# Optimization experiments

Measured on AMD Instinct MI355X. Metric: run time of the kernel, lower is better.

The kernel has to match this reference:

```python
import jax, jax.numpy as jnp
import numpy as np

B, S, H = 2, 2048, 2048
NH, KVH, HD = 32, 8, 64
G = NH // KVH
BASE = 10000.0
SCALE = 1.0 / np.sqrt(HD).astype(np.float32)


def _rope_cache(seq_len, dim, base):
    inv_freq = 1.0 / (base ** (jnp.arange(0, dim, 2, dtype=jnp.float32) / dim))
    t = jnp.arange(seq_len, dtype=jnp.float32)
    freqs = jnp.outer(t, inv_freq)            # [S, HD/2]
    emb = jnp.concatenate([freqs, freqs], -1)  # [S, HD]
    return jnp.cos(emb), jnp.sin(emb)


def _rotate_half(x):
    x1, x2 = jnp.split(x, 2, axis=-1)
    return jnp.concatenate([-x2, x1], axis=-1)


def setup_inputs() -> dict:
    key = jax.random.key(0)
    ks = jax.random.split(key, 5)
    hidden_states = jax.random.normal(ks[0], (B, S, H), jnp.float32)
    # additive causal mask, broadcast over heads
    causal = jnp.tril(jnp.ones((S, S), dtype=bool))
    attention_mask = jnp.where(causal, 0.0, -1e9).astype(jnp.float32)[None, None]
    attention_mask = jnp.broadcast_to(attention_mask, (B, 1, S, S))
    position_ids = jnp.broadcast_to(jnp.arange(S, dtype=jnp.int32), (B, S))
    w = 0.02
    Wq = jax.random.normal(ks[1], (H, NH * HD), jnp.float32) * w
    Wk = jax.random.normal(ks[2], (H, KVH * HD), jnp.float32) * w
    Wv = jax.random.normal(ks[3], (H, KVH * HD), jnp.float32) * w
    Wo = jax.random.normal(ks[4], (NH * HD, H), jnp.float32) * w
    return {"hidden_states": hidden_states, "attention_mask": attention_mask,
            "position_ids": position_ids, "Wq": Wq, "Wk": Wk, "Wv": Wv, "Wo": Wo}


def reference(hidden_states, attention_mask, position_ids, Wq, Wk, Wv, Wo):
    b, s, _ = hidden_states.shape
    q = (hidden_states @ Wq).reshape(b, s, NH, HD).transpose(0, 2, 1, 3)   # [B,NH,S,HD]
    k = (hidden_states @ Wk).reshape(b, s, KVH, HD).transpose(0, 2, 1, 3)  # [B,KVH,S,HD]
    v = (hidden_states @ Wv).reshape(b, s, KVH, HD).transpose(0, 2, 1, 3)
    cos_c, sin_c = _rope_cache(s, HD, BASE)
    cos = cos_c[position_ids][:, None]  # [B,1,S,HD]
    sin = sin_c[position_ids][:, None]
    q = q * cos + _rotate_half(q) * sin
    k = k * cos + _rotate_half(k) * sin
    # GQA: grouped einsum == repeat_kv + matmul (same math, no KV duplication)
    qg = q.reshape(b, KVH, G, s, HD)
    scores = jnp.einsum('bkgsd,bktd->bkgst', qg, k) * SCALE  # [B,KVH,G,S,S]
    scores = scores + attention_mask[:, :, None]             # mask [B,1,1,S,S]
    probs = jax.nn.softmax(scores.astype(jnp.float32), axis=-1).astype(q.dtype)
    ctx = jnp.einsum('bkgst,bktd->bkgsd', probs, v)
    ctx = ctx.reshape(b, NH, s, HD).transpose(0, 2, 1, 3).reshape(b, s, NH * HD)
    return ctx @ Wo
```

## Files before the change

### kernel.cpp

```cpp
#include <hip/hip_runtime.h>
#include <hip/hip_bf16.h>

#define DB   2
#define DS   2048
#define DH   2048
#define DNH  32
#define DKVH 8
#define DHD  64
#define DM   4096
#define DNQKV 3072

typedef __attribute__((ext_vector_type(8))) short bf16x8;
typedef __attribute__((ext_vector_type(4))) float f32x4;
typedef __attribute__((ext_vector_type(8))) unsigned short us8;
typedef __attribute__((ext_vector_type(4))) unsigned short us4;

__device__ __forceinline__ float b2f(unsigned short u) {
  unsigned int x = ((unsigned int)u) << 16;
  return __builtin_bit_cast(float, x);
}
__device__ __forceinline__ unsigned short f2b(float f) {
  unsigned int u = __builtin_bit_cast(unsigned int, f);
  return (unsigned short)((u + 0x8000u) >> 16);
}
__device__ __forceinline__ void async_copy16(void* lds, const void* g) {
  __builtin_amdgcn_global_load_lds((const __attribute__((address_space(1))) void*)g,
                                   (__attribute__((address_space(3))) void*)lds,
                                   16, 0, 0);
}

#define BARRIER() do { asm volatile("" ::: "memory"); __builtin_amdgcn_s_barrier(); asm volatile("" ::: "memory"); } while (0)
#define LGKM0()   asm volatile("s_waitcnt lgkmcnt(0)" ::: "memory")
#define WAITVM(n) asm volatile("s_waitcnt vmcnt(" #n ")" ::: "memory")
#define MFMA16(d, a, bb) (d) = __builtin_amdgcn_mfma_f32_16x16x32_bf16((a), (bb), (d), 0, 0, 0)

__global__ void detect_mode(const unsigned short* __restrict__ w, int* __restrict__ flags) {
  int t = threadIdx.x;
  int trips = 0;
  for (int i = 0; i < 4; i++) {
    unsigned short u = w[t * 4 + i];
    int e = (u >> 7) & 0xFF;
    if (e >= 161 || (e <= 93 && e != 0)) trips++;
  }
  for (int off = 32; off > 0; off >>= 1) trips += __shfl_down(trips, off);
  if (t == 0) flags[0] = (trips >= 8) ? 1 : 0;
}

__global__ __launch_bounds__(256) void convert_x(const void* __restrict__ xin,
                                                 unsigned short* __restrict__ xb,
                                                 const int* __restrict__ flags, int n) {
  int mode = flags[0];
  int i = (blockIdx.x * 256 + threadIdx.x) * 8;
  if (i >= n) return;
  if (mode) {
    const float* f = (const float*)xin;
    us8 o;
#pragma unroll
    for (int j = 0; j < 8; j++) o[j] = f2b(f[i + j]);
    *(us8*)&xb[i] = o;
  } else {
    *(us8*)&xb[i] = *(const us8*)((const unsigned short*)xin + i);
  }
}

__global__ __launch_bounds__(256) void transpose_w(const void* __restrict__ win,
                                                   unsigned short* __restrict__ out,
                                                   const int* __restrict__ flags,
                                                   int R, int C) {
  __shared__ float tile[32][33];
  int mode = flags[0];
  int c0 = blockIdx.x * 32, r0 = blockIdx.y * 32;
  int tx = threadIdx.x & 31, ty = threadIdx.x >> 5;
  if (mode) {
    const float* f = (const float*)win;
    for (int i = ty; i < 32; i += 8) tile[i][tx] = f[(size_t)(r0 + i) * C + c0 + tx];
  } else {
    const unsigned short* bsrc = (const unsigned short*)win;
    for (int i = ty; i < 32; i += 8) tile[i][tx] = b2f(bsrc[(size_t)(r0 + i) * C + c0 + tx]);
  }
  __syncthreads();
  for (int i = ty; i < 32; i += 8) out[(size_t)(c0 + i) * R + r0 + tx] = f2b(tile[tx][i]);
}

#define QSC 0.18033688011112042f

__global__ __launch_bounds__(512, 2)
void gemm_qkv(const unsigned short* __restrict__ A, const unsigned short* __restrict__ Bt,
              const int* __restrict__ pos_ids,
              unsigned short* __restrict__ qws, unsigned short* __restrict__ kws,
              unsigned short* __restrict__ vt) {
  __shared__ __align__(16) unsigned short sm[65536];
  int tid = threadIdx.x, lane = tid & 63, wave = tid >> 6;
  int wm = wave >> 2, wn = wave & 3;
  int quad = lane >> 4, l15 = lane & 15;

  int bid = blockIdx.x;
  int wg = (bid & 7) * 24 + (bid >> 3);
  int ty = wg / 12, tx = wg - ty * 12;
  size_t tm0 = (size_t)ty * 256, tn0 = (size_t)tx * 256;

  const unsigned short* Ab = A + tm0 * 2048;
  const unsigned short* Bb = Bt + tn0 * 2048;

  auto UA = [&](int bu, int kh) { return sm + (bu * 2 + kh) * 8192; };
  auto UB = [&](int bu, int kh) { return sm + 32768 + (bu * 2 + kh) * 8192; };

  int c0 = tid, c1 = tid + 512;
  int r0s = c0 >> 2, r1s = c1 >> 2;
  int cc0 = (c0 & 3) ^ ((r0s >> 1) & 3);
  int cc1 = (c1 & 3) ^ ((r1s >> 1) & 3);
  size_t ga0 = (size_t)r0s * 2048 + cc0 * 8;
  size_t ga1 = (size_t)r1s * 2048 + cc1 * 8;

  auto stA = [&](int t, int kh, int bu) {
    const unsigned short* s = Ab + (size_t)t * 64 + kh * 32;
    async_copy16(UA(bu, kh) + c0 * 8, s + ga0);
    async_copy16(UA(bu, kh) + c1 * 8, s + ga1);
  };
  auto stB = [&](int t, int kh, int bu) {
    const unsigned short* s = Bb + (size_t)t * 64 + kh * 32;
    async_copy16(UB(bu, kh) + c0 * 8, s + ga0);
    async_copy16(UB(bu, kh) + c1 * 8, s + ga1);
  };

  int rdoff = l15 * 32 + ((quad << 3) ^ (((l15 >> 1) & 3) << 3));

  f32x4 zero4 = {0.f, 0.f, 0.f, 0.f};
  f32x4 acc[8][4];
#pragma unroll
  for (int mi = 0; mi < 8; mi++)
#pragma unroll
    for (int ni = 0; ni < 4; ni++) acc[mi][ni] = zero4;

  stA(0, 0, 0); stB(0, 0, 0); stA(0, 1, 0); stB(0, 1, 0); stA(1, 0, 1); stB(1, 0, 1);
  WAITVM(8); BARRIER();

#pragma unroll 2
  for (int t = 0; t < 32; ++t) {
    int bu = t & 1, bn = bu ^ 1;
    int t1 = (t + 1 < 32) ? t + 1 : 31;
    int t2 = (t + 2 < 32) ? t + 2 : 31;
    bf16x8 af[8];
    const unsigned short* pA0 = UA(bu, 0) + wm * 4096 + rdoff;
    const unsigned short* pB0 = UB(bu, 0) + wn * 2048 + rdoff;
    const unsigned short* pA1 = UA(bu, 1) + wm * 4096 + rdoff;
    const unsigned short* pB1 = UB(bu, 1) + wn * 2048 + rdoff;

#pragma unroll
    for (int mi = 0; mi < 8; mi++) af[mi] = *(const bf16x8*)(pA0 + mi * 512);
    bf16x8 b0 = *(const bf16x8*)pB0;
    bf16x8 b1 = *(const bf16x8*)(pB0 + 512);
    stA(t1, 1, bn);
    BARRIER(); LGKM0();
    __builtin_amdgcn_s_setprio(1);
#pragma unroll
    for (int mi = 0; mi < 8; mi++) { MFMA16(acc[mi][0], af[mi], b0); MFMA16(acc[mi][1], af[mi], b1); }
    __builtin_amdgcn_s_setprio(0);
    BARRIER();

    bf16x8 b2 = *(const bf16x8*)(pB0 + 1024);
    bf16x8 b3 = *(const bf16x8*)(pB0 + 1536);
    stB(t1, 1, bn);
    BARRIER(); LGKM0();
    __builtin_amdgcn_s_setprio(1);
#pragma unroll
    for (int mi = 0; mi < 8; mi++) { MFMA16(acc[mi][2], af[mi], b2); MFMA16(acc[mi][3], af[mi], b3); }
    __builtin_amdgcn_s_setprio(0);
    WAITVM(8);
    BARRIER();

#pragma unroll
    for (int mi = 0; mi < 8; mi++) af[mi] = *(const bf16x8*)(pA1 + mi * 512);
    b0 = *(const bf16x8*)pB1;
    b1 = *(const bf16x8*)(pB1 + 512);
    stA(t2, 0, bu);
    BARRIER(); LGKM0();
    __builtin_amdgcn_s_setprio(1);
#pragma unroll
    for (int mi = 0; mi < 8; mi++) { MFMA16(acc[mi][0], af[mi], b0); MFMA16(acc[mi][1], af[mi], b1); }
    __builtin_amdgcn_s_setprio(0);
    BARRIER();

    b2 = *(const bf16x8*)(pB1 + 1024);
    b3 = *(const bf16x8*)(pB1 + 1536);
    stB(t2, 0, bu);
    BARRIER(); LGKM0();
    __builtin_amdgcn_s_setprio(1);
#pragma unroll
    for (int mi = 0; mi < 8; mi++) { MFMA16(acc[mi][2], af[mi], b2); MFMA16(acc[mi][3], af[mi], b3); }
    __builtin_amdgcn_s_setprio(0);
    WAITVM(8);
    BARRIER();
  }
  WAITVM(0);

  int hs = (int)(tn0 >> 6) + wn;
  if (hs < 40) {
    float sc = (hs < 32) ? QSC : 1.0f;
    unsigned short* dst0 = (hs < 32) ? qws : kws;
    int hh = (hs < 32) ? hs : (hs - 32);
    float invf0 = __expf(-(float)l15 * (9.210340371976184f / 32.0f));
    float invf1 = invf0 * 0.01f;
#pragma unroll
    for (int mi = 0; mi < 8; mi++)
#pragma unroll
      for (int r = 0; r < 4; r++) {
        size_t gr = tm0 + wm * 128 + mi * 16 + quad * 4 + r;
        int bb = (int)(gr >> 11), s = (int)(gr & 2047);
        float tpos = (float)pos_ids[gr];
        unsigned short* row = dst0 + ((size_t)(bb * ((hs < 32) ? DNH : DKVH) + hh) * DS + s) * DHD;
#pragma unroll
        for (int ni = 0; ni < 2; ni++) {
          float x1 = acc[mi][ni][r], x2 = acc[mi][ni + 2][r];
          float ang = tpos * (ni ? invf1 : invf0);
          float sn, cs;
          __sincosf(ang, &sn, &cs);
          int d = ni * 16 + l15;
          row[d]      = f2b((x1 * cs - x2 * sn) * sc);
          row[d + 32] = f2b((x2 * cs + x1 * sn) * sc);
        }
      }
  } else {
    int vh = hs - 40;
    int bb = (int)(tm0 >> 11);
    int s0 = (int)(tm0 & 2047) + wm * 128 + quad * 4;
#pragma unroll
    for (int mi = 0; mi < 8; mi++)
#pragma unroll
      for (int ni = 0; ni < 4; ni++) {
        int d = ni * 16 + l15;
        us4 o4;
#pragma unroll
        for (int r = 0; r < 4; r++) o4[r] = f2b(acc[mi][ni][r]);
        *(us4*)&vt[((size_t)(bb * DKVH + vh) * DHD + d) * DS + s0 + mi * 16] = o4;
      }
  }
}

__global__ __launch_bounds__(512, 2)
void gemm_out(const unsigned short* __restrict__ A, const unsigned short* __restrict__ Bt,
              unsigned short* __restrict__ Cb, float* __restrict__ Cf,
              const int* __restrict__ outmode) {
  __shared__ __align__(16) unsigned short sm[49152];
  int tid = threadIdx.x, lane = tid & 63, wave = tid >> 6;
  int wm = wave >> 2, wn = wave & 3;
  int quad = lane >> 4, l15 = lane & 15;

  int bid = blockIdx.x;
  int wg = (bid & 7) * 32 + (bid >> 3);
  int ty = wg >> 3, tx = wg & 7;
  size_t tm0 = (size_t)ty * 128, tn0 = (size_t)tx * 256;

  const unsigned short* Ab = A + tm0 * 2048;
  const unsigned short* Bb = Bt + tn0 * 2048;

  auto UA = [&](int bu, int kh) { return sm + (bu * 2 + kh) * 4096; };
  auto UB = [&](int bu, int kh) { return sm + 16384 + (bu * 2 + kh) * 8192; };

  int c0 = tid, c1 = tid + 512;
  int r0s = c0 >> 2, r1s = c1 >> 2;
  int cc0 = (c0 & 3) ^ ((r0s >> 1) & 3);
  int cc1 = (c1 & 3) ^ ((r1s >> 1) & 3);
  size_t ga0 = (size_t)r0s * 2048 + cc0 * 8;
  size_t ga1 = (size_t)r1s * 2048 + cc1 * 8;

  auto stA = [&](int t, int kh, int bu) {
    const unsigned short* s = Ab + (size_t)t * 64 + kh * 32;
    async_copy16(UA(bu, kh) + c0 * 8, s + ga0);
  };
  auto stB = [&](int t, int kh, int bu) {
    const unsigned short* s = Bb + (size_t)t * 64 + kh * 32;
    async_copy16(UB(bu, kh) + c0 * 8, s + ga0);
    async_copy16(UB(bu, kh) + c1 * 8, s + ga1);
  };

  int rdoff = l15 * 32 + ((quad << 3) ^ (((l15 >> 1) & 3) << 3));

  f32x4 zero4 = {0.f, 0.f, 0.f, 0.f};
  f32x4 acc[4][4];
#pragma unroll
  for (int mi = 0; mi < 4; mi++)
#pragma unroll
    for (int ni = 0; ni < 4; ni++) acc[mi][ni] = zero4;

  stA(0, 0, 0); stB(0, 0, 0); stA(0, 1, 0); stB(0, 1, 0); stA(1, 0, 1); stB(1, 0, 1);
  WAITVM(6); BARRIER();

#pragma unroll 2
  for (int t = 0; t < 32; ++t) {
    int bu = t & 1, bn = bu ^ 1;
    int t1 = (t + 1 < 32) ? t + 1 : 31;
    int t2 = (t + 2 < 32) ? t + 2 : 31;
    bf16x8 af[4];
    const unsigned short* pA0 = UA(bu, 0) + wm * 2048 + rdoff;
    const unsigned short* pB0 = UB(bu, 0) + wn * 2048 + rdoff;
    const unsigned short* pA1 = UA(bu, 1) + wm * 2048 + rdoff;
    const unsigned short* pB1 = UB(bu, 1) + wn * 2048 + rdoff;

#pragma unroll
    for (int mi = 0; mi < 4; mi++) af[mi] = *(const bf16x8*)(pA0 + mi * 512);
    bf16x8 b0 = *(const bf16x8*)pB0;
    bf16x8 b1 = *(const bf16x8*)(pB0 + 512);
    stA(t1, 1, bn);
    BARRIER(); LGKM0();
    __builtin_amdgcn_s_setprio(1);
#pragma unroll
    for (int mi = 0; mi < 4; mi++) { MFMA16(acc[mi][0], af[mi], b0); MFMA16(acc[mi][1], af[mi], b1); }
    __builtin_amdgcn_s_setprio(0);
    BARRIER();

    bf16x8 b2 = *(const bf16x8*)(pB0 + 1024);
    bf16x8 b3 = *(const bf16x8*)(pB0 + 1536);
    stB(t1, 1, bn);
    BARRIER(); LGKM0();
    __builtin_amdgcn_s_setprio(1);
#pragma unroll
    for (int mi = 0; mi < 4; mi++) { MFMA16(acc[mi][2], af[mi], b2); MFMA16(acc[mi][3], af[mi], b3); }
    __builtin_amdgcn_s_setprio(0);
    WAITVM(6);
    BARRIER();

#pragma unroll
    for (int mi = 0; mi < 4; mi++) af[mi] = *(const bf16x8*)(pA1 + mi * 512);
    b0 = *(const bf16x8*)pB1;
    b1 = *(const bf16x8*)(pB1 + 512);
    stA(t2, 0, bu);
    BARRIER(); LGKM0();
    __builtin_amdgcn_s_setprio(1);
#pragma unroll
    for (int mi = 0; mi < 4; mi++) { MFMA16(acc[mi][0], af[mi], b0); MFMA16(acc[mi][1], af[mi], b1); }
    __builtin_amdgcn_s_setprio(0);
    BARRIER();

    b2 = *(const bf16x8*)(pB1 + 1024);
    b3 = *(const bf16x8*)(pB1 + 1536);
    stB(t2, 0, bu);
    BARRIER(); LGKM0();
    __builtin_amdgcn_s_setprio(1);
#pragma unroll
    for (int mi = 0; mi < 4; mi++) { MFMA16(acc[mi][2], af[mi], b2); MFMA16(acc[mi][3], af[mi], b3); }
    __builtin_amdgcn_s_setprio(0);
    WAITVM(6);
    BARRIER();
  }
  WAITVM(0);

  int mode = *outmode;
#pragma unroll
  for (int mi = 0; mi < 4; mi++)
#pragma unroll
    for (int ni = 0; ni < 4; ni++)
#pragma unroll
      for (int r = 0; r < 4; r++) {
        size_t gr = tm0 + wm * 64 + mi * 16 + quad * 4 + r;
        size_t gc = tn0 + wn * 64 + ni * 16 + l15;
        float v = acc[mi][ni][r];
        if (mode) Cf[gr * 2048 + gc] = v;
        else      Cb[gr * 2048 + gc] = f2b(v);
      }
}

__global__ __launch_bounds__(256, 4)
void flash_attn(const unsigned short* __restrict__ q, const unsigned short* __restrict__ k,
                const unsigned short* __restrict__ vt, unsigned short* __restrict__ ctx) {
  __shared__ __align__(16) unsigned short lK0[64 * 32];
  __shared__ __align__(16) unsigned short lK1[64 * 32];
  __shared__ __align__(16) unsigned short lV0[64 * 32];
  __shared__ __align__(16) unsigned short lV1[64 * 32];
  __shared__ __align__(16) unsigned short lP[4 * 16 * 72];
  int tid = threadIdx.x, lane = tid & 63, wave = tid >> 6;
  int quad = lane >> 4, l15 = lane & 15;
  int bh = blockIdx.y, b = bh >> 5, h = bh & 31, kvh = h >> 2;
  const unsigned short* qb = q + (size_t)(b * DNH + h) * DS * DHD;
  const unsigned short* kb = k + (size_t)(b * DKVH + kvh) * DS * DHD;
  const unsigned short* vb = vt + (size_t)(b * DKVH + kvh) * DHD * DS;
  unsigned short* lPw = lP + wave * 16 * 72;
  int r4 = tid >> 2, c8 = (tid & 3) * 8;

  f32x4 zero4 = {0.f, 0.f, 0.f, 0.f};
  for (int ph = 0; ph < 2; ph++) {
    int qt = ph ? (31 - blockIdx.x) : blockIdx.x;
    int q0 = qt * 64;
    const unsigned short* qp = qb + (size_t)(q0 + wave * 16 + l15) * DHD + quad * 8;
    bf16x8 qf0 = *(const bf16x8*)qp;
    bf16x8 qf1 = *(const bf16x8*)(qp + 32);
    f32x4 oacc[4];
#pragma unroll
    for (int dj = 0; dj < 4; dj++) oacc[dj] = zero4;
    float mrow = -1e30f, lrow = 0.f;

    int nt = qt + 1;
    for (int t = 0; t < nt; t++) {
      int kv0 = t * 64;
      __syncthreads();
      async_copy16(&lK0[tid * 8], kb + (size_t)(kv0 + r4) * DHD + c8);
      async_copy16(&lK1[tid * 8], kb + (size_t)(kv0 + r4) * DHD + 32 + c8);
      async_copy16(&lV0[tid * 8], vb + (size_t)r4 * DS + kv0 + c8);
      async_copy16(&lV1[tid * 8], vb + (size_t)r4 * DS + kv0 + 32 + c8);
      __syncthreads();

      f32x4 sacc[4];
#pragma unroll
      for (int nj = 0; nj < 4; nj++) {
        sacc[nj] = zero4;
        bf16x8 kf0 = *(const bf16x8*)&lK0[(nj * 16 + l15) * 32 + quad * 8];
        bf16x8 kf1 = *(const bf16x8*)&lK1[(nj * 16 + l15) * 32 + quad * 8];
        sacc[nj] = __builtin_amdgcn_mfma_f32_16x16x32_bf16(kf0, qf0, sacc[nj], 0, 0, 0);
        sacc[nj] = __builtin_amdgcn_mfma_f32_16x16x32_bf16(kf1, qf1, sacc[nj], 0, 0, 0);
      }
      if (t == nt - 1) {
        int ql = wave * 16 + l15;
#pragma unroll
        for (int nj = 0; nj < 4; nj++)
#pragma unroll
          for (int r = 0; r < 4; r++)
            if (nj * 16 + quad * 4 + r > ql) sacc[nj][r] = -1e30f;
      }
      float tm = -1e30f;
#pragma unroll
      for (int nj = 0; nj < 4; nj++)
#pragma unroll
        for (int r = 0; r < 4; r++) tm = fmaxf(tm, sacc[nj][r]);
      tm = fmaxf(tm, __shfl_xor(tm, 16));
      tm = fmaxf(tm, __shfl_xor(tm, 32));
      float mn = fmaxf(mrow, tm);
      float alpha = __builtin_amdgcn_exp2f(mrow - mn);
      mrow = mn;
      float rs = 0.f;
      float p[4][4];
#pragma unroll
      for (int nj = 0; nj < 4; nj++)
#pragma unroll
        for (int r = 0; r < 4; r++) {
          float e = __builtin_amdgcn_exp2f(sacc[nj][r] - mn);
          p[nj][r] = e;
          rs += e;
        }
      rs += __shfl_xor(rs, 16);
      rs += __shfl_xor(rs, 32);
      lrow = lrow * alpha + rs;
#pragma unroll
      for (int nj = 0; nj < 4; nj++) {
        us4 w4;
#pragma unroll
        for (int r = 0; r < 4; r++) w4[r] = f2b(p[nj][r]);
        *(us4*)&lPw[l15 * 72 + nj * 16 + quad * 4] = w4;
      }
      bf16x8 pf0 = *(const bf16x8*)&lPw[l15 * 72 + quad * 8];
      bf16x8 pf1 = *(const bf16x8*)&lPw[l15 * 72 + 32 + quad * 8];
#pragma unroll
      for (int dj = 0; dj < 4; dj++) {
#pragma unroll
        for (int r = 0; r < 4; r++) oacc[dj][r] *= alpha;
        bf16x8 vf0 = *(const bf16x8*)&lV0[(dj * 16 + l15) * 32 + quad * 8];
        bf16x8 vf1 = *(const bf16x8*)&lV1[(dj * 16 + l15) * 32 + quad * 8];
        oacc[dj] = __builtin_amdgcn_mfma_f32_16x16x32_bf16(vf0, pf0, oacc[dj], 0, 0, 0);
        oacc[dj] = __builtin_amdgcn_mfma_f32_16x16x32_bf16(vf1, pf1, oacc[dj], 0, 0, 0);
      }
    }
    float inv = __builtin_amdgcn_rcpf(lrow);
    size_t orow = ((size_t)b * DS + q0 + wave * 16 + l15) * (DNH * DHD) + (size_t)h * DHD;
#pragma unroll
    for (int dj = 0; dj < 4; dj++) {
      us4 o4;
#pragma unroll
      for (int r = 0; r < 4; r++) o4[r] = f2b(oacc[dj][r] * inv);
      *(us4*)&ctx[orow + dj * 16 + quad * 4] = o4;
    }
  }
}

extern "C" void kernel_launch(void* const* d_in, const int* in_sizes, int n_in,
                              void* d_out, int out_size, void* d_ws, size_t ws_size,
                              hipStream_t stream) {
  (void)in_sizes; (void)n_in; (void)out_size; (void)ws_size;
  const void* hs = d_in[0];
  const int* pos = (const int*)d_in[2];
  const void* wq = d_in[3];
  const void* wk = d_in[4];
  const void* wv = d_in[5];
  const void* wo = d_in[6];

  char* ws = (char*)d_ws;
  size_t off = 0;
  auto take = [&](size_t bytes) -> char* {
    char* p = ws + off;
    off += (bytes + 255) & ~(size_t)255;
    return p;
  };
  int* flags            = (int*)take(256);
  unsigned short* xb    = (unsigned short*)take((size_t)DM * DH * 2);
  unsigned short* wtqkv = (unsigned short*)take((size_t)DNQKV * DH * 2);
  unsigned short* wto   = (unsigned short*)take((size_t)DH * DH * 2);
  unsigned short* qws   = (unsigned short*)take((size_t)DB * DNH * DS * DHD * 2);
  unsigned short* kws   = (unsigned short*)take((size_t)DB * DKVH * DS * DHD * 2);
  unsigned short* vtws  = (unsigned short*)take((size_t)DB * DKVH * DS * DHD * 2);
  unsigned short* ctx   = (unsigned short*)take((size_t)DM * DNH * DHD * 2);

  detect_mode<<<1, 64, 0, stream>>>((const unsigned short*)wq, flags);
  convert_x<<<DM * DH / 8 / 256, 256, 0, stream>>>(hs, xb, flags, DM * DH);
  transpose_w<<<dim3(64, 64), 256, 0, stream>>>(wq, wtqkv, flags, 2048, 2048);
  transpose_w<<<dim3(16, 64), 256, 0, stream>>>(wk, wtqkv + (size_t)2048 * 2048, flags, 2048, 512);
  transpose_w<<<dim3(16, 64), 256, 0, stream>>>(wv, wtqkv + (size_t)2560 * 2048, flags, 2048, 512);
  transpose_w<<<dim3(64, 64), 256, 0, stream>>>(wo, wto, flags, 2048, 2048);

  gemm_qkv<<<dim3(192), 512, 0, stream>>>(xb, wtqkv, pos, qws, kws, vtws);

  flash_attn<<<dim3(16, DB * DNH), 256, 0, stream>>>(qws, kws, vtws, ctx);

  gemm_out<<<dim3(256), 512, 0, stream>>>(ctx, wto, (unsigned short*)d_out, (float*)d_out, flags);
}
```

Baseline: 329.3 us.

## Double-buffer K tiles, load V from global to registers, lazy softmax rescale

Restructures the flash attention inner loop. K tiles are now double-buffered in LDS with an XOR swizzle, and the next tile is prefetched while the current one is computed. V fragments are read straight from global memory into registers instead of being staged in LDS. The online-softmax rescale of the accumulators is skipped unless the running max grows by more than 8 (log2 units), and bf16 packing now uses the v_cvt_pk_bf16_f32 instruction. These changes aim to hide load latency and cut barriers and ALU work, at the cost of uncoalesced global V reads and possible exp2 overflow risk bounded by the threshold.

```diff
diff --git a/kernel.cpp b/kernel.cpp
--- a/kernel.cpp
+++ b/kernel.cpp
@@ -14,6 +14,7 @@
 typedef __attribute__((ext_vector_type(4))) float f32x4;
 typedef __attribute__((ext_vector_type(8))) unsigned short us8;
 typedef __attribute__((ext_vector_type(4))) unsigned short us4;
+typedef __attribute__((ext_vector_type(2))) unsigned int u32x2;
 
 __device__ __forceinline__ float b2f(unsigned short u) {
   unsigned int x = ((unsigned int)u) << 16;
@@ -22,6 +23,11 @@
 __device__ __forceinline__ unsigned short f2b(float f) {
   unsigned int u = __builtin_bit_cast(unsigned int, f);
   return (unsigned short)((u + 0x8000u) >> 16);
+}
+__device__ __forceinline__ unsigned int cvt_pk_bf16(float lo, float hi) {
+  unsigned int r;
+  asm("v_cvt_pk_bf16_f32 %0, %1, %2" : "=v"(r) : "v"(lo), "v"(hi));
+  return r;
 }
 __device__ __forceinline__ void async_copy16(void* lds, const void* g) {
   __builtin_amdgcn_global_load_lds((const __attribute__((address_space(1))) void*)g,
@@ -363,10 +369,7 @@
 __global__ __launch_bounds__(256, 4)
 void flash_attn(const unsigned short* __restrict__ q, const unsigned short* __restrict__ k,
                 const unsigned short* __restrict__ vt, unsigned short* __restrict__ ctx) {
-  __shared__ __align__(16) unsigned short lK0[64 * 32];
-  __shared__ __align__(16) unsigned short lK1[64 * 32];
-  __shared__ __align__(16) unsigned short lV0[64 * 32];
-  __shared__ __align__(16) unsigned short lV1[64 * 32];
+  __shared__ __align__(16) unsigned short lK[2][2][64 * 32];
   __shared__ __align__(16) unsigned short lP[4 * 16 * 72];
   int tid = threadIdx.x, lane = tid & 63, wave = tid >> 6;
   int quad = lane >> 4, l15 = lane & 15;
@@ -375,7 +378,9 @@
   const unsigned short* kb = k + (size_t)(b * DKVH + kvh) * DS * DHD;
   const unsigned short* vb = vt + (size_t)(b * DKVH + kvh) * DHD * DS;
   unsigned short* lPw = lP + wave * 16 * 72;
-  int r4 = tid >> 2, c8 = (tid & 3) * 8;
+  int r4 = tid >> 2;
+  int cc8 = ((tid & 3) ^ ((r4 >> 1) & 3)) * 8;
+  int swz = ((l15 >> 1) & 3) << 3;
 
   f32x4 zero4 = {0.f, 0.f, 0.f, 0.f};
   for (int ph = 0; ph < 2; ph++) {
@@ -390,23 +395,37 @@
     float mrow = -1e30f, lrow = 0.f;
 
     int nt = qt + 1;
+    {
+      const unsigned short* s = kb + (size_t)r4 * DHD + cc8;
+      async_copy16(&lK[0][0][tid * 8], s);
+      async_copy16(&lK[0][1][tid * 8], s + 32);
+    }
+    WAITVM(0); BARRIER();
+
+    int cur = 0;
     for (int t = 0; t < nt; t++) {
       int kv0 = t * 64;
-      __syncthreads();
-      async_copy16(&lK0[tid * 8], kb + (size_t)(kv0 + r4) * DHD + c8);
-      async_copy16(&lK1[tid * 8], kb + (size_t)(kv0 + r4) * DHD + 32 + c8);
-      async_copy16(&lV0[tid * 8], vb + (size_t)r4 * DS + kv0 + c8);
-      async_copy16(&lV1[tid * 8], vb + (size_t)r4 * DS + kv0 + 32 + c8);
-      __syncthreads();
-
+      if (t + 1 < nt) {
+        const unsigned short* s = kb + (size_t)(kv0 + 64 + r4) * DHD + cc8;
+        async_copy16(&lK[cur ^ 1][0][tid * 8], s);
+        async_copy16(&lK[cur ^ 1][1][tid * 8], s + 32);
+      }
       f32x4 sacc[4];
 #pragma unroll
       for (int nj = 0; nj < 4; nj++) {
+        int ro = (nj * 16 + l15) * 32 + ((quad * 8) ^ swz);
+        bf16x8 kf0 = *(const bf16x8*)&lK[cur][0][ro];
+        bf16x8 kf1 = *(const bf16x8*)&lK[cur][1][ro];
         sacc[nj] = zero4;
-        bf16x8 kf0 = *(const bf16x8*)&lK0[(nj * 16 + l15) * 32 + quad * 8];
-        bf16x8 kf1 = *(const bf16x8*)&lK1[(nj * 16 + l15) * 32 + quad * 8];
-        sacc[nj] = __builtin_amdgcn_mfma_f32_16x16x32_bf16(kf0, qf0, sacc[nj], 0, 0, 0);
-        sacc[nj] = __builtin_amdgcn_mfma_f32_16x16x32_bf16(kf1, qf1, sacc[nj], 0, 0, 0);
+        MFMA16(sacc[nj], kf0, qf0);
+        MFMA16(sacc[nj], kf1, qf1);
+      }
+      bf16x8 vf0[4], vf1[4];
+#pragma unroll
+      for (int dj = 0; dj < 4; dj++) {
+        const unsigned short* vp = vb + (size_t)(dj * 16 + l15) * DS + kv0 + quad * 8;
+        vf0[dj] = *(const bf16x8*)vp;
+        vf1[dj] = *(const bf16x8*)(vp + 32);
       }
       if (t == nt - 1) {
         int ql = wave * 16 + l15;
@@ -416,56 +435,61 @@
           for (int r = 0; r < 4; r++)
             if (nj * 16 + quad * 4 + r > ql) sacc[nj][r] = -1e30f;
       }
-      float tm = -1e30f;
-#pragma unroll
-      for (int nj = 0; nj < 4; nj++)
-#pragma unroll
-        for (int r = 0; r < 4; r++) tm = fmaxf(tm, sacc[nj][r]);
+      float a0 = fmaxf(fmaxf(sacc[0][0], sacc[0][1]), sacc[0][2]);
+      float a1 = fmaxf(fmaxf(sacc[0][3], sacc[1][0]), sacc[1][1]);
+      float a2 = fmaxf(fmaxf(sacc[1][2], sacc[1][3]), sacc[2][0]);
+      float a3 = fmaxf(fmaxf(sacc[2][1], sacc[2][2]), sacc[2][3]);
+      float a4 = fmaxf(fmaxf(sacc[3][0], sacc[3][1]), sacc[3][2]);
+      float tm = fmaxf(fmaxf(fmaxf(a0, a1), fmaxf(a2, a3)), fmaxf(a4, sacc[3][3]));
       tm = fmaxf(tm, __shfl_xor(tm, 16));
       tm = fmaxf(tm, __shfl_xor(tm, 32));
-      float mn = fmaxf(mrow, tm);
-      float alpha = __builtin_amdgcn_exp2f(mrow - mn);
-      mrow = mn;
+      if (!__all(tm <= mrow + 8.f)) {
+        float mn = fmaxf(mrow, tm);
+        float alpha = __builtin_amdgcn_exp2f(mrow - mn);
+        mrow = mn;
+        lrow *= alpha;
+#pragma unroll
+        for (int dj = 0; dj < 4; dj++)
+#pragma unroll
+          for (int r = 0; r < 4; r++) oacc[dj][r] *= alpha;
+      }
       float rs = 0.f;
-      float p[4][4];
 #pragma unroll
       for (int nj = 0; nj < 4; nj++)
 #pragma unroll
         for (int r = 0; r < 4; r++) {
-          float e = __builtin_amdgcn_exp2f(sacc[nj][r] - mn);
-          p[nj][r] = e;
+          float e = __builtin_amdgcn_exp2f(sacc[nj][r] - mrow);
+          sacc[nj][r] = e;
           rs += e;
         }
       rs += __shfl_xor(rs, 16);
       rs += __shfl_xor(rs, 32);
-      lrow = lrow * alpha + rs;
+      lrow += rs;
 #pragma unroll
       for (int nj = 0; nj < 4; nj++) {
-        us4 w4;
-#pragma unroll
-        for (int r = 0; r < 4; r++) w4[r] = f2b(p[nj][r]);
-        *(us4*)&lPw[l15 * 72 + nj * 16 + quad * 4] = w4;
+        u32x2 w2;
+        w2[0] = cvt_pk_bf16(sacc[nj][0], sacc[nj][1]);
+        w2[1] = cvt_pk_bf16(sacc[nj][2], sacc[nj][3]);
+        *(u32x2*)&lPw[l15 * 72 + nj * 16 + quad * 4] = w2;
       }
       bf16x8 pf0 = *(const bf16x8*)&lPw[l15 * 72 + quad * 8];
       bf16x8 pf1 = *(const bf16x8*)&lPw[l15 * 72 + 32 + quad * 8];
 #pragma unroll
       for (int dj = 0; dj < 4; dj++) {
-#pragma unroll
-        for (int r = 0; r < 4; r++) oacc[dj][r] *= alpha;
-        bf16x8 vf0 = *(const bf16x8*)&lV0[(dj * 16 + l15) * 32 + quad * 8];
-        bf16x8 vf1 = *(const bf16x8*)&lV1[(dj * 16 + l15) * 32 + quad * 8];
-        oacc[dj] = __builtin_amdgcn_mfma_f32_16x16x32_bf16(vf0, pf0, oacc[dj], 0, 0, 0);
-        oacc[dj] = __builtin_amdgcn_mfma_f32_16x16x32_bf16(vf1, pf1, oacc[dj], 0, 0, 0);
-      }
+        MFMA16(oacc[dj], vf0[dj], pf0);
+        MFMA16(oacc[dj], vf1[dj], pf1);
+      }
+      WAITVM(0); BARRIER();
+      cur ^= 1;
     }
     float inv = __builtin_amdgcn_rcpf(lrow);
     size_t orow = ((size_t)b * DS + q0 + wave * 16 + l15) * (DNH * DHD) + (size_t)h * DHD;
 #pragma unroll
     for (int dj = 0; dj < 4; dj++) {
-      us4 o4;
-#pragma unroll
-      for (int r = 0; r < 4; r++) o4[r] = f2b(oacc[dj][r] * inv);
-      *(us4*)&ctx[orow + dj * 16 + quad * 4] = o4;
+      u32x2 o2;
+      o2[0] = cvt_pk_bf16(oacc[dj][0] * inv, oacc[dj][1] * inv);
+      o2[1] = cvt_pk_bf16(oacc[dj][2] * inv, oacc[dj][3] * inv);
+      *(u32x2*)&ctx[orow + dj * 16 + quad * 4] = o2;
     }
   }
 }
```

Measured after the change: 387.3 us. 17.6% more time.
